# Kernel tuning notes

Hardware: AMD Instinct MI355X
Metric: run time of the kernel (lower is better)

## Reference

```python
import jax, jax.numpy as jnp
import numpy as np

B, S, HID, NH, FF, K = 2, 2048, 1024, 16, 4096, 512
DH = HID // NH


def setup_inputs() -> dict:
    key = jax.random.key(0)
    ks = jax.random.split(key, 24)
    w = lambda k, shape: (jax.random.normal(k, shape, jnp.float32) * 0.02)
    inp = {
        'x': jax.random.normal(ks[0], (B, S, HID), jnp.float32),
        'mask': jnp.ones((B, 1, 1, S), jnp.int32),
        'Wq': w(ks[1], (HID, HID)), 'bq': jnp.zeros((HID,), jnp.float32),
        'Wk': w(ks[2], (HID, HID)), 'bk': jnp.zeros((HID,), jnp.float32),
        'Wv': w(ks[3], (HID, HID)), 'bv': jnp.zeros((HID,), jnp.float32),
        'Wo': w(ks[4], (HID, HID)), 'bo': jnp.zeros((HID,), jnp.float32),
        'rel_emb': w(ks[5], (2 * K, HID)),
        'Wpk': w(ks[6], (HID, HID)), 'bpk': jnp.zeros((HID,), jnp.float32),
        'Wpq': w(ks[7], (HID, HID)), 'bpq': jnp.zeros((HID,), jnp.float32),
        'ln1_g': jnp.ones((HID,), jnp.float32), 'ln1_b': jnp.zeros((HID,), jnp.float32),
        'ln2_g': jnp.ones((HID,), jnp.float32), 'ln2_b': jnp.zeros((HID,), jnp.float32),
        'W1': w(ks[8], (HID, FF)), 'b1': jnp.zeros((FF,), jnp.float32),
        'W2': w(ks[9], (FF, HID)), 'b2': jnp.zeros((HID,), jnp.float32),
    }
    return inp


def _layernorm(x, g, b, eps=1e-6):
    m = jnp.mean(x, -1, keepdims=True)
    v = jnp.mean(jnp.square(x - m), -1, keepdims=True)
    return (x - m) * jax.lax.rsqrt(v + eps) * g + b


def _disentangled_attention(x, mask, Wq, bq, Wk, bk, Wv, bv, Wo, bo,
                            rel_emb, Wpk, bpk, Wpq, bpq):
    # content projections -> [B, NH, S, DH]
    def heads(t):
        return t.reshape(B, S, NH, DH).transpose(0, 2, 1, 3)
    q = heads(x @ Wq + bq)
    k = heads(x @ Wk + bk)
    v = heads(x @ Wv + bv)

    # relative position index: rel[i, j] = clip(i - j, -K, K-1) + K in [0, 2K)
    pos = jnp.arange(S)
    rel = jnp.clip(pos[:, None] - pos[None, :], -K, K - 1) + K  # [S, S]

    # projected relative-position embeddings -> [2K, NH, DH]
    pos_k = (rel_emb @ Wpk + bpk).reshape(2 * K, NH, DH)
    pos_q = (rel_emb @ Wpq + bpq).reshape(2 * K, NH, DH)

    # content-to-content
    c2c = jnp.einsum('bhid,bhjd->bhij', q, k)
    # content-to-position: gather over relative bucket per (i, j)
    c2p_att = jnp.einsum('bhid,rhd->bhir', q, pos_k)               # [B,NH,S,2K]
    c2p = jnp.take_along_axis(c2p_att, rel[None, None, :, :], axis=-1)
    # position-to-content: K_j . Q_r[delta(j, i)], gather then transpose
    p2c_att = jnp.einsum('bhjd,rhd->bhjr', k, pos_q)               # [B,NH,S,2K]
    p2c = jnp.take_along_axis(p2c_att, rel[None, None, :, :], axis=-1)
    p2c = p2c.transpose(0, 1, 3, 2)

    scale = 1.0 / jnp.sqrt(jnp.asarray(3 * DH, jnp.float32))
    scores = (c2c + c2p + p2c) * scale                             # [B,NH,S,S]
    scores = jnp.where(mask == 0, jnp.asarray(-1e9, scores.dtype), scores)
    attn = jax.nn.softmax(scores, axis=-1)

    out = jnp.einsum('bhij,bhjd->bhid', attn, v)
    out = out.transpose(0, 2, 1, 3).reshape(B, S, HID)
    return out @ Wo + bo


def reference(x, mask, Wq, bq, Wk, bk, Wv, bv, Wo, bo, rel_emb, Wpk, bpk,
              Wpq, bpq, ln1_g, ln1_b, ln2_g, ln2_b, W1, b1, W2, b2):
    # pre-norm sublayer 1: x + attn(LN(x))
    h = x + _disentangled_attention(_layernorm(x, ln1_g, ln1_b), mask,
                                    Wq, bq, Wk, bk, Wv, bv, Wo, bo,
                                    rel_emb, Wpk, bpk, Wpq, bpq)
    # pre-norm sublayer 2: h + FFN(LN(h)), GELU activation
    hn = _layernorm(h, ln2_g, ln2_b)
    ff = jax.nn.gelu(hn @ W1 + b1) @ W2 + b2
    return h + ff
```

## Files before the change

### kernel.cpp

```cpp
#include <hip/hip_runtime.h>
#include <cstdint>
#include <cstddef>

#define DEV __device__ __forceinline__

typedef __attribute__((ext_vector_type(4))) float  f32x4;
typedef __attribute__((ext_vector_type(4))) float  float4v;
typedef __attribute__((ext_vector_type(8))) short  s16x8;
typedef __attribute__((ext_vector_type(4))) short  s16x4;

static constexpr int BB = 2, SS = 2048, HIDN = 1024, NHH = 16, FFN = 4096, DH = 64;
static constexpr int TWOK = 1024;
static constexpr int HG = 8;
static constexpr float ATT_SCALE = 0.07216878364870322f;

DEV short f2bf(float f) {
  union { float f; uint32_t u; } v; v.f = f;
  uint32_t r = (v.u + 0x7fffu + ((v.u >> 16) & 1u)) >> 16;
  return (short)r;
}
DEV float bfu(unsigned short u) {
  union { uint32_t u; float f; } v; v.u = ((uint32_t)u) << 16; return v.f;
}
DEV int imin(int a, int b) { return a < b ? a : b; }
DEV int imax(int a, int b) { return a > b ? a : b; }

DEV void gl_lds16(const void* g, void* l) {
  __builtin_amdgcn_global_load_lds((const __attribute__((address_space(1))) void*)g,
                                   (__attribute__((address_space(3))) void*)l, 16, 0, 0);
}

#define MFMA16(a, b, c) __builtin_amdgcn_mfma_f32_16x16x32_bf16((a), (b), (c), 0, 0, 0)

__global__ __launch_bounds__(256) void k_tcast(const float* __restrict__ in,
                                               short* __restrict__ out, int R, int C) {
  __shared__ float t[32][33];
  const int bx = blockIdx.x * 32, by = blockIdx.y * 32;
  const int tx = threadIdx.x & 31, ty = threadIdx.x >> 5;
#pragma unroll
  for (int r = ty; r < 32; r += 8) t[r][tx] = in[(size_t)(by + r) * C + bx + tx];
  __syncthreads();
#pragma unroll
  for (int c = ty; c < 32; c += 8) out[(size_t)(bx + c) * R + by + tx] = f2bf(t[tx][c]);
}

struct TCBatch { const float* in[5]; short* out[5]; };
__global__ __launch_bounds__(256) void k_tcast5(TCBatch tc) {
  __shared__ float t[32][33];
  const float* in = tc.in[blockIdx.z];
  short* out = tc.out[blockIdx.z];
  const int bx = blockIdx.x * 32, by = blockIdx.y * 32;
  const int tx = threadIdx.x & 31, ty = threadIdx.x >> 5;
#pragma unroll
  for (int r = ty; r < 32; r += 8) t[r][tx] = in[(size_t)(by + r) * 1024 + bx + tx];
  __syncthreads();
#pragma unroll
  for (int c = ty; c < 32; c += 8) out[(size_t)(bx + c) * 1024 + by + tx] = f2bf(t[tx][c]);
}

__global__ __launch_bounds__(256) void k_cast(const float* __restrict__ in,
                                              short* __restrict__ out, int n4) {
  const int i = blockIdx.x * 256 + threadIdx.x;
  if (i < n4) {
    float4v v = ((const float4v*)in)[i];
    s16x4 o; o[0] = f2bf(v.x); o[1] = f2bf(v.y); o[2] = f2bf(v.z); o[3] = f2bf(v.w);
    ((s16x4*)out)[i] = o;
  }
}

__global__ __launch_bounds__(256) void k_ln(const float* __restrict__ x,
                                            const float* __restrict__ gw,
                                            const float* __restrict__ bw,
                                            short* __restrict__ out) {
  const int row = blockIdx.x, t = threadIdx.x, lane = t & 63, wv = t >> 6;
  __shared__ float red[8];
  const float4v v = ((const float4v*)(x + (size_t)row * HIDN))[t];
  float s = v.x + v.y + v.z + v.w;
#pragma unroll
  for (int d = 1; d < 64; d <<= 1) s += __shfl_xor(s, d, 64);
  if (lane == 0) red[wv] = s;
  __syncthreads();
  const float mean = (red[0] + red[1] + red[2] + red[3]) * (1.f / 1024.f);
  const float dx = v.x - mean, dy = v.y - mean, dz = v.z - mean, dw = v.w - mean;
  float s2 = dx * dx + dy * dy + dz * dz + dw * dw;
#pragma unroll
  for (int d = 1; d < 64; d <<= 1) s2 += __shfl_xor(s2, d, 64);
  if (lane == 0) red[4 + wv] = s2;
  __syncthreads();
  const float var = (red[4] + red[5] + red[6] + red[7]) * (1.f / 1024.f);
  const float rs = rsqrtf(var + 1e-6f);
  const float4v g4 = ((const float4v*)gw)[t], b4 = ((const float4v*)bw)[t];
  s16x4 o;
  o[0] = f2bf(dx * rs * g4.x + b4.x);
  o[1] = f2bf(dy * rs * g4.y + b4.y);
  o[2] = f2bf(dz * rs * g4.z + b4.z);
  o[3] = f2bf(dw * rs * g4.w + b4.w);
  ((s16x4*)(out + (size_t)row * HIDN))[t] = o;
}

DEV void gemm_main(const short* __restrict__ A, const short* __restrict__ Bt, int K,
                   int m0, int n0, int tid, int wm, int wn, int lr, int lg,
                   short* As, short* Bs, f32x4 acc[4][4]) {
  for (int k0 = 0; k0 < K; k0 += 32) {
#pragma unroll
    for (int c = tid; c < 512; c += 256) {
      const int row = c >> 2, col = (c & 3) * 8;
      gl_lds16(A + (size_t)(m0 + row) * K + k0 + col, (char*)As + c * 16);
      gl_lds16(Bt + (size_t)(n0 + row) * K + k0 + col, (char*)Bs + c * 16);
    }
    __syncthreads();
    s16x8 af[4], bf[4];
#pragma unroll
    for (int fi = 0; fi < 4; ++fi) af[fi] = *(const s16x8*)&As[(wm + fi * 16 + lr) * 32 + lg * 8];
#pragma unroll
    for (int fj = 0; fj < 4; ++fj) bf[fj] = *(const s16x8*)&Bs[(wn + fj * 16 + lr) * 32 + lg * 8];
#pragma unroll
    for (int fi = 0; fi < 4; ++fi)
#pragma unroll
      for (int fj = 0; fj < 4; ++fj) acc[fi][fj] = MFMA16(af[fi], bf[fj], acc[fi][fj]);
    __syncthreads();
  }
}

enum { OM_GELU = 0, OM_RESID = 1 };

template <int OM>
__global__ __launch_bounds__(256) void k_gemm(const short* __restrict__ A,
                                              const short* __restrict__ Bt,
                                              const float* __restrict__ bias,
                                              const float* __restrict__ resid,
                                              void* __restrict__ out,
                                              int M, int N, int K) {
  __shared__ short As[128 * 32];
  __shared__ short Bs[128 * 32];
  const int tid = threadIdx.x, lane = tid & 63, wave = tid >> 6;
  const int m0 = blockIdx.y * 128, n0 = blockIdx.x * 128;
  const int wm = (wave >> 1) * 64, wn = (wave & 1) * 64;
  const int lr = lane & 15, lg = lane >> 4;

  f32x4 acc[4][4];
#pragma unroll
  for (int i = 0; i < 4; ++i)
#pragma unroll
    for (int j = 0; j < 4; ++j) acc[i][j] = (f32x4){0.f, 0.f, 0.f, 0.f};
  gemm_main(A, Bt, K, m0, n0, tid, wm, wn, lr, lg, As, Bs, acc);

#pragma unroll
  for (int fi = 0; fi < 4; ++fi)
#pragma unroll
    for (int fj = 0; fj < 4; ++fj) {
      const int n = n0 + wn + fj * 16 + lr;
      const float bv = bias[n];
#pragma unroll
      for (int r = 0; r < 4; ++r) {
        const int m = m0 + wm + fi * 16 + lg * 4 + r;
        float v = acc[fi][fj][r] + bv;
        if constexpr (OM == OM_GELU) {
          const float z = 0.7978845608028654f * (v + 0.044715f * v * v * v);
          const float th = 1.f - 2.f / (1.f + __expf(2.f * z));
          ((short*)out)[(size_t)m * N + n] = f2bf(0.5f * v * (1.f + th));
        } else {
          ((float*)out)[(size_t)m * N + n] = v + resid[(size_t)m * N + n];
        }
      }
    }
}

__global__ __launch_bounds__(256) void k_gemm_qkv(const short* __restrict__ A,
                                                  const short* __restrict__ Bt,
                                                  const float* __restrict__ bq,
                                                  const float* __restrict__ bk,
                                                  const float* __restrict__ bv,
                                                  short* __restrict__ qo,
                                                  short* __restrict__ ko,
                                                  short* __restrict__ vo) {
  __shared__ short As[128 * 32];
  __shared__ short Bs[128 * 32];
  const int tid = threadIdx.x, lane = tid & 63, wave = tid >> 6;
  const int m0 = blockIdx.y * 128, n0 = blockIdx.x * 128;
  const int wm = (wave >> 1) * 64, wn = (wave & 1) * 64;
  const int lr = lane & 15, lg = lane >> 4;

  f32x4 acc[4][4];
#pragma unroll
  for (int i = 0; i < 4; ++i)
#pragma unroll
    for (int j = 0; j < 4; ++j) acc[i][j] = (f32x4){0.f, 0.f, 0.f, 0.f};
  gemm_main(A, Bt, 1024, m0, n0, tid, wm, wn, lr, lg, As, Bs, acc);

#pragma unroll
  for (int fi = 0; fi < 4; ++fi)
#pragma unroll
    for (int fj = 0; fj < 4; ++fj) {
      const int n = n0 + wn + fj * 16 + lr;
      const int proj = n >> 10, nn = n & 1023;
      const int hh = nn >> 6, dd = nn & 63;
      const float bvv = (proj == 0 ? bq : proj == 1 ? bk : bv)[nn];
#pragma unroll
      for (int r = 0; r < 4; ++r) {
        const int m = m0 + wm + fi * 16 + lg * 4 + r;
        const int b = m >> 11, s = m & (SS - 1);
        const float v = acc[fi][fj][r] + bvv;
        if (proj == 2)
          vo[(((size_t)b * NHH + hh) * DH + dd) * SS + s] = f2bf(v);
        else
          (proj == 0 ? qo : ko)[(((size_t)b * NHH + hh) * SS + s) * DH + dd] = f2bf(v);
      }
    }
}

__global__ __launch_bounds__(256) void k_gemm_pos(const short* __restrict__ A,
                                                  const short* __restrict__ Bt,
                                                  const float* __restrict__ bpk,
                                                  const float* __restrict__ bpq,
                                                  short* __restrict__ pko,
                                                  short* __restrict__ pqo) {
  __shared__ short As[128 * 32];
  __shared__ short Bs[128 * 32];
  const int tid = threadIdx.x, lane = tid & 63, wave = tid >> 6;
  const int m0 = blockIdx.y * 128, n0 = blockIdx.x * 128;
  const int wm = (wave >> 1) * 64, wn = (wave & 1) * 64;
  const int lr = lane & 15, lg = lane >> 4;

  f32x4 acc[4][4];
#pragma unroll
  for (int i = 0; i < 4; ++i)
#pragma unroll
    for (int j = 0; j < 4; ++j) acc[i][j] = (f32x4){0.f, 0.f, 0.f, 0.f};
  gemm_main(A, Bt, 1024, m0, n0, tid, wm, wn, lr, lg, As, Bs, acc);

#pragma unroll
  for (int fi = 0; fi < 4; ++fi)
#pragma unroll
    for (int fj = 0; fj < 4; ++fj) {
      const int n = n0 + wn + fj * 16 + lr;
      const int pos = n >> 10, nn = n & 1023;
      const int hh = nn >> 6, dd = nn & 63;
      const float bvv = (pos == 0 ? bpk : bpq)[nn];
      short* ob = pos == 0 ? pko : pqo;
#pragma unroll
      for (int r = 0; r < 4; ++r) {
        const int m = m0 + wm + fi * 16 + lg * 4 + r;
        ob[((size_t)hh * TWOK + m) * DH + dd] = f2bf(acc[fi][fj][r] + bvv);
      }
    }
}

__global__ __launch_bounds__(256) void k_posgemm(const short* __restrict__ qh,
                                                 const short* __restrict__ kh,
                                                 const short* __restrict__ posk,
                                                 const short* __restrict__ posq,
                                                 short* __restrict__ c2pO,
                                                 short* __restrict__ p2cD,
                                                 short* __restrict__ p2cE, int h0) {
  __shared__ short As[128 * 64];
  __shared__ short Bs[128 * 64];
  __shared__ short L[128 * 129];
  const int tid = threadIdx.x, lane = tid & 63, wave = tid >> 6;
  const int z = blockIdx.z;
  const int hl = z & (HG - 1), b = (z >> 3) & 1, isP = z >> 4;
  const int h = h0 + hl;
  const int bhl = b * HG + hl;
  const int m0 = blockIdx.y * 128, n0 = blockIdx.x * 128;
  const int wm = (wave >> 1) * 64, wn = (wave & 1) * 64;
  const int lr = lane & 15, lg = lane >> 4;
  const short* Ab = (isP ? kh : qh) + ((size_t)b * NHH + h) * SS * DH;
  const short* Pb = (isP ? posq : posk) + (size_t)h * TWOK * DH;

#pragma unroll
  for (int c = tid; c < 1024; c += 256) {
    const int row = c >> 3, col = (c & 7) * 8;
    gl_lds16(Ab + (size_t)(m0 + row) * DH + col, (char*)As + c * 16);
    gl_lds16(Pb + (size_t)(n0 + row) * DH + col, (char*)Bs + c * 16);
  }
  __syncthreads();

  f32x4 acc[4][4];
#pragma unroll
  for (int i = 0; i < 4; ++i)
#pragma unroll
    for (int j = 0; j < 4; ++j) acc[i][j] = (f32x4){0.f, 0.f, 0.f, 0.f};

#pragma unroll
  for (int ks = 0; ks < 2; ++ks) {
    s16x8 af[4], bf[4];
#pragma unroll
    for (int fi = 0; fi < 4; ++fi) af[fi] = *(const s16x8*)&As[(wm + fi * 16 + lr) * 64 + ks * 32 + lg * 8];
#pragma unroll
    for (int fj = 0; fj < 4; ++fj) bf[fj] = *(const s16x8*)&Bs[(wn + fj * 16 + lr) * 64 + ks * 32 + lg * 8];
#pragma unroll
    for (int fi = 0; fi < 4; ++fi)
#pragma unroll
      for (int fj = 0; fj < 4; ++fj) acc[fi][fj] = MFMA16(af[fi], bf[fj], acc[fi][fj]);
  }

  if (!isP) {
    short* ob = c2pO + (size_t)bhl * SS * TWOK;
#pragma unroll
    for (int fi = 0; fi < 4; ++fi)
#pragma unroll
      for (int fj = 0; fj < 4; ++fj) {
        const int n = n0 + wn + fj * 16 + lr;
#pragma unroll
        for (int r = 0; r < 4; ++r) {
          const int m = m0 + wm + fi * 16 + lg * 4 + r;
          ob[(size_t)m * TWOK + n] = f2bf(acc[fi][fj][r]);
        }
      }
  } else {
#pragma unroll
    for (int fi = 0; fi < 4; ++fi)
#pragma unroll
      for (int fj = 0; fj < 4; ++fj) {
        const int n = n0 + wn + fj * 16 + lr;
        const int nl = n - n0;
#pragma unroll
        for (int r = 0; r < 4; ++r) {
          const int m = m0 + wm + fi * 16 + lg * 4 + r;
          const int ml = m - m0;
          const short val = f2bf(acc[fi][fj][r]);
          L[ml * 129 + nl] = val;
          if (n == 0)        p2cE[((size_t)bhl * 2 + 0) * SS + m] = val;
          if (n == TWOK - 1) p2cE[((size_t)bhl * 2 + 1) * SS + m] = val;
        }
      }
    __syncthreads();
    const int nl = tid & 127, ty = tid >> 7;
    const int ibase = m0 - n0 + 385;
    short* pD = p2cD + (size_t)bhl * SS * TWOK;
    for (int p = 0; p < 128; ++p) {
      const int il = p * 2 + ty;
      if (il < 255) {
        const int ml = nl + il - 127;
        const int ig = ibase + il;
        if (ml >= 0 && ml < 128 && ig >= 0 && ig < SS)
          pD[(size_t)ig * TWOK + n0 + nl] = L[ml * 129 + nl];
      }
    }
  }
}

__global__ __launch_bounds__(256) void k_attn(const short* __restrict__ qh,
                                              const short* __restrict__ kh,
                                              const short* __restrict__ vT,
                                              const short* __restrict__ c2p,
                                              const short* __restrict__ p2cD,
                                              const short* __restrict__ p2cE,
                                              const int* __restrict__ mask,
                                              short* __restrict__ ao, int h0) {
  __shared__ char smem[4 * 16 * 68 * 4];
  __shared__ float Mm[4][16];
  __shared__ float Lm[4][16];
  float (*Om)[16][68] = (float(*)[16][68])smem;
  short (*Ps)[16][72] = (short(*)[16][72])smem;

  const int tid = threadIdx.x, lane = tid & 63, wv = tid >> 6;
  const int lr = lane & 15, lg = lane >> 4;

  const int bid = blockIdx.x;
  const int itile = bid & 127;
  const int hl = (bid >> 7) & (HG - 1);
  const int b = bid >> 10;
  const int h = h0 + hl;
  const int i0 = itile * 16;
  const size_t bhoff = ((size_t)b * NHH + h) * SS * DH;
  const size_t bhl = (size_t)b * HG + hl;
  const int jq0 = wv * (SS / 4);

  const short* qrow = qh + bhoff + (size_t)(i0 + lr) * DH + lg * 8;
  const s16x8 qa0 = *(const s16x8*)qrow;
  const s16x8 qa1 = *(const s16x8*)(qrow + 32);

  const unsigned short* c2prow[4];
  float cLoV[4], cHiV[4];
#pragma unroll
  for (int r = 0; r < 4; ++r) {
    c2prow[r] = (const unsigned short*)(c2p + (bhl * SS + (size_t)(i0 + lg * 4 + r)) * TWOK);
    cLoV[r] = bfu(c2prow[r][0]);
    cHiV[r] = bfu(c2prow[r][TWOK - 1]);
  }
  const ptrdiff_t pdelta = (const char*)p2cD - (const char*)c2p;
  const unsigned short* pE0 = (const unsigned short*)(p2cE + (bhl * 2 + 0) * SS);
  const unsigned short* pE1 = (const unsigned short*)(p2cE + (bhl * 2 + 1) * SS);

  const int dbase = i0 + lg * 4 - lr;

  f32x4 oacc[4];
  float mprev[4], lsum[4];
#pragma unroll
  for (int r = 0; r < 4; ++r) {
    mprev[r] = -1e30f; lsum[r] = 0.f; oacc[r] = (f32x4){0.f, 0.f, 0.f, 0.f};
  }

  for (int jt = 0; jt < SS / 4 / 64; ++jt) {
    const int j0 = jq0 + jt * 64;
    const int d0 = i0 - j0;

    f32x4 sacc[4];
#pragma unroll
    for (int fj = 0; fj < 4; ++fj) {
      const short* krow = kh + bhoff + (size_t)(j0 + fj * 16 + lr) * DH + lg * 8;
      const s16x8 k0 = *(const s16x8*)krow;
      const s16x8 k1 = *(const s16x8*)(krow + 32);
      f32x4 a = (f32x4){0.f, 0.f, 0.f, 0.f};
      a = MFMA16(qa0, k0, a);
      a = MFMA16(qa1, k1, a);
      sacc[fj] = a;
    }

    float pvv[4][4];
    if (d0 >= 576) {
#pragma unroll
      for (int fj = 0; fj < 4; ++fj) {
        const int jl = fj * 16 + lr;
        const bool ok = mask[(size_t)b * SS + j0 + jl] != 0;
        const float pe = bfu(pE0[j0 + jl]);
#pragma unroll
        for (int r = 0; r < 4; ++r) {
          const float s = (sacc[fj][r] + cHiV[r] + pe) * ATT_SCALE;
          pvv[fj][r] = ok ? s : -1e9f;
        }
      }
    } else if (d0 <= -528) {
#pragma unroll
      for (int fj = 0; fj < 4; ++fj) {
        const int jl = fj * 16 + lr;
        const bool ok = mask[(size_t)b * SS + j0 + jl] != 0;
        const float pe = bfu(pE1[j0 + jl]);
#pragma unroll
        for (int r = 0; r < 4; ++r) {
          const float s = (sacc[fj][r] + cLoV[r] + pe) * ATT_SCALE;
          pvv[fj][r] = ok ? s : -1e9f;
        }
      }
    } else {
#pragma unroll
      for (int fj = 0; fj < 4; ++fj) {
        const int jl = fj * 16 + lr;
        const bool ok = mask[(size_t)b * SS + j0 + jl] != 0;
        const float pe0 = bfu(pE0[j0 + jl]);
        const float pe1 = bfu(pE1[j0 + jl]);
        const int dl0 = dbase - fj * 16 - j0;
#pragma unroll
        for (int r = 0; r < 4; ++r) {
          const int dl = dl0 + r;
          const int cc = imin(imax(dl + 512, 0), 1023);
          const int raw = 512 - dl;
          const int cp = imin(imax(raw, 0), 1023);
          const unsigned short* pDrow =
              (const unsigned short*)((const char*)c2prow[r] + pdelta);
          float p2cv = bfu(pDrow[cp]);
          p2cv = raw < 0 ? pe0 : p2cv;
          p2cv = raw > 1023 ? pe1 : p2cv;
          const float s = (sacc[fj][r] + bfu(c2prow[r][cc]) + p2cv) * ATT_SCALE;
          pvv[fj][r] = ok ? s : -1e9f;
        }
      }
    }

#pragma unroll
    for (int r = 0; r < 4; ++r) {
      float m = fmaxf(fmaxf(pvv[0][r], pvv[1][r]), fmaxf(pvv[2][r], pvv[3][r]));
#pragma unroll
      for (int dd = 1; dd < 16; dd <<= 1) m = fmaxf(m, __shfl_xor(m, dd, 64));
      const float mnew = fmaxf(mprev[r], m);
      const float corr = __expf(mprev[r] - mnew);
      float rs = 0.f;
#pragma unroll
      for (int fj = 0; fj < 4; ++fj) { pvv[fj][r] = __expf(pvv[fj][r] - mnew); rs += pvv[fj][r]; }
#pragma unroll
      for (int dd = 1; dd < 16; dd <<= 1) rs += __shfl_xor(rs, dd, 64);
      lsum[r] = lsum[r] * corr + rs;
      mprev[r] = mnew;
#pragma unroll
      for (int fd = 0; fd < 4; ++fd) oacc[fd][r] *= corr;
    }

#pragma unroll
    for (int fj = 0; fj < 4; ++fj)
#pragma unroll
      for (int r = 0; r < 4; ++r)
        Ps[wv][lg * 4 + r][fj * 16 + lr] = f2bf(pvv[fj][r]);

    const s16x8 pa0 = *(const s16x8*)&Ps[wv][lr][lg * 8];
    const s16x8 pa1 = *(const s16x8*)&Ps[wv][lr][32 + lg * 8];
#pragma unroll
    for (int fd = 0; fd < 4; ++fd) {
      const short* vrow = vT + bhoff + (size_t)(fd * 16 + lr) * SS + j0 + lg * 8;
      const s16x8 v0 = *(const s16x8*)vrow;
      const s16x8 v1 = *(const s16x8*)(vrow + 32);
      oacc[fd] = MFMA16(pa0, v0, oacc[fd]);
      oacc[fd] = MFMA16(pa1, v1, oacc[fd]);
    }
  }

  __syncthreads();
#pragma unroll
  for (int fd = 0; fd < 4; ++fd)
#pragma unroll
    for (int r = 0; r < 4; ++r)
      Om[wv][lg * 4 + r][fd * 16 + lr] = oacc[fd][r];
  if (lr == 0) {
#pragma unroll
    for (int r = 0; r < 4; ++r) { Mm[wv][lg * 4 + r] = mprev[r]; Lm[wv][lg * 4 + r] = lsum[r]; }
  }
  __syncthreads();

#pragma unroll
  for (int r = 0; r < 4; ++r) {
    const int il = lg * 4 + r;
    float mt = fmaxf(fmaxf(Mm[0][il], Mm[1][il]), fmaxf(Mm[2][il], Mm[3][il]));
    float L = 0.f, o = 0.f;
#pragma unroll
    for (int w = 0; w < 4; ++w) {
      const float sc = __expf(Mm[w][il] - mt);
      L += Lm[w][il] * sc;
      o += Om[w][il][wv * 16 + lr] * sc;
    }
    ao[((size_t)b * SS + i0 + il) * HIDN + h * DH + wv * 16 + lr] = f2bf(o / L);
  }
}

extern "C" void kernel_launch(void* const* d_in, const int* in_sizes, int n_in,
                              void* d_out, int out_size, void* d_ws, size_t ws_size,
                              hipStream_t stream) {
  const float* x   = (const float*)d_in[0];
  const int* mask  = (const int*)d_in[1];
  const float* Wq  = (const float*)d_in[2];  const float* bq  = (const float*)d_in[3];
  const float* Wk  = (const float*)d_in[4];  const float* bk  = (const float*)d_in[5];
  const float* Wv  = (const float*)d_in[6];  const float* bv  = (const float*)d_in[7];
  const float* Wo  = (const float*)d_in[8];  const float* bo  = (const float*)d_in[9];
  const float* rel = (const float*)d_in[10];
  const float* Wpk = (const float*)d_in[11]; const float* bpk = (const float*)d_in[12];
  const float* Wpq = (const float*)d_in[13]; const float* bpq = (const float*)d_in[14];
  const float* g1  = (const float*)d_in[15]; const float* be1 = (const float*)d_in[16];
  const float* g2  = (const float*)d_in[17]; const float* be2 = (const float*)d_in[18];
  const float* W1  = (const float*)d_in[19]; const float* bf1 = (const float*)d_in[20];
  const float* W2  = (const float*)d_in[21]; const float* bf2 = (const float*)d_in[22];
  float* out = (float*)d_out;

  char* ws = (char*)d_ws;
  const size_t MB = (size_t)1 << 20;
  short* aoB   = (short*)(ws + 0 * MB);
  short* qhB   = (short*)(ws + 8 * MB);
  short* khB   = (short*)(ws + 16 * MB);
  short* vTB   = (short*)(ws + 24 * MB);
  short* poskB = (short*)(ws + 32 * MB);
  short* posqB = (short*)(ws + 34 * MB);
  short* xn    = (short*)(ws + 36 * MB);
  short* WqT   = (short*)(ws + 44 * MB);
  short* WkT   = (short*)(ws + 46 * MB);
  short* WvT   = (short*)(ws + 48 * MB);
  short* WpkT  = (short*)(ws + 50 * MB);
  short* WpqT  = (short*)(ws + 52 * MB);
  short* relbf = (short*)(ws + 54 * MB);
  short* c2pG  = (short*)(ws + 36 * MB);
  short* p2cDG = (short*)(ws + 100 * MB);
  short* p2cE  = (short*)(ws + 164 * MB);
  short* WoT   = (short*)(ws + 36 * MB);
  short* hnB   = (short*)(ws + 38 * MB);
  short* W1T   = (short*)(ws + 46 * MB);
  short* W2T   = (short*)(ws + 54 * MB);
  short* midB  = (short*)(ws + 62 * MB);
  (void)ws_size; (void)in_sizes; (void)n_in; (void)out_size;

  const int M = BB * SS;

  TCBatch tc;
  tc.in[0] = Wq;  tc.out[0] = WqT;
  tc.in[1] = Wk;  tc.out[1] = WkT;
  tc.in[2] = Wv;  tc.out[2] = WvT;
  tc.in[3] = Wpk; tc.out[3] = WpkT;
  tc.in[4] = Wpq; tc.out[4] = WpqT;
  k_tcast5<<<dim3(32, 32, 5), 256, 0, stream>>>(tc);
  k_cast<<<1024, 256, 0, stream>>>(rel, relbf, 1024 * 1024 / 4);
  k_ln<<<M, 256, 0, stream>>>(x, g1, be1, xn);

  k_gemm_qkv<<<dim3(24, 32), 256, 0, stream>>>(xn, WqT, bq, bk, bv, qhB, khB, vTB);
  k_gemm_pos<<<dim3(16, 8), 256, 0, stream>>>(relbf, WpkT, bpk, bpq, poskB, posqB);

  for (int g = 0; g < NHH / HG; ++g) {
    const int h0 = g * HG;
    k_posgemm<<<dim3(8, 16, 4 * HG), 256, 0, stream>>>(qhB, khB, poskB, posqB,
                                                       c2pG, p2cDG, p2cE, h0);
    k_attn<<<BB * HG * 128, 256, 0, stream>>>(qhB, khB, vTB, c2pG, p2cDG, p2cE, mask, aoB, h0);
  }

  k_tcast<<<dim3(32, 32), 256, 0, stream>>>(Wo, WoT, 1024, 1024);
  k_gemm<OM_RESID><<<dim3(8, 32), 256, 0, stream>>>(aoB, WoT, bo, x, out, M, 1024, 1024);
  k_ln<<<M, 256, 0, stream>>>(out, g2, be2, hnB);
  k_tcast<<<dim3(128, 32), 256, 0, stream>>>(W1, W1T, 1024, 4096);
  k_tcast<<<dim3(32, 128), 256, 0, stream>>>(W2, W2T, 4096, 1024);
  k_gemm<OM_GELU><<<dim3(32, 32), 256, 0, stream>>>(hnB, W1T, bf1, nullptr, midB, M, 4096, 1024);
  k_gemm<OM_RESID><<<dim3(8, 32), 256, 0, stream>>>(midB, W2T, bf2, out, out, M, 1024, 4096);
}
```

Measured before the change: 723.2 us.

## Process 32 query rows per attention block and vectorize p2c diagonal scatter

The attention kernel now handles two 16-row query sub-tiles per block, so each K and V fragment load is reused across 32 rows and the grid is halved. The p2c diagonal scatter in the position GEMM now writes 8 contiguous shorts per thread with vector stores instead of scalar per-element stores. In exchange, register pressure rises from doubled accumulators, which may reduce occupancy, and the far-low threshold changed from -528 to -544.

```diff
diff --git a/kernel.cpp b/kernel.cpp
--- a/kernel.cpp
+++ b/kernel.cpp
@@ -325,16 +325,33 @@
         }
       }
     __syncthreads();
-    const int nl = tid & 127, ty = tid >> 7;
+    const int ty = tid >> 4;
+    const int cx = (tid & 15) * 8;
     const int ibase = m0 - n0 + 385;
     short* pD = p2cD + (size_t)bhl * SS * TWOK;
-    for (int p = 0; p < 128; ++p) {
-      const int il = p * 2 + ty;
-      if (il < 255) {
-        const int ml = nl + il - 127;
-        const int ig = ibase + il;
-        if (ml >= 0 && ml < 128 && ig >= 0 && ig < SS)
-          pD[(size_t)ig * TWOK + n0 + nl] = L[ml * 129 + nl];
+    for (int p = 0; p < 16; ++p) {
+      const int il = p * 16 + ty;
+      if (il >= 255) continue;
+      const int ig = ibase + il;
+      if (ig < 0 || ig >= SS) continue;
+      const int lo = imax(0, 127 - il), hi = imin(127, 254 - il);
+      if (cx > hi || cx + 7 < lo) continue;
+      short* dst = pD + (size_t)ig * TWOK + n0 + cx;
+      const int mlb = cx + il - 127;
+      if (cx >= lo && cx + 7 <= hi) {
+        s16x4 t0, t1;
+#pragma unroll
+        for (int q = 0; q < 4; ++q) t0[q] = L[(mlb + q) * 129 + cx + q];
+#pragma unroll
+        for (int q = 0; q < 4; ++q) t1[q] = L[(mlb + 4 + q) * 129 + cx + 4 + q];
+        *(s16x4*)dst = t0;
+        *(s16x4*)(dst + 4) = t1;
+      } else {
+#pragma unroll
+        for (int q = 0; q < 8; ++q) {
+          const int nl = cx + q;
+          if (nl >= lo && nl <= hi) dst[q] = L[(mlb + q) * 129 + nl];
+        }
       }
     }
   }
@@ -348,177 +365,222 @@
                                               const short* __restrict__ p2cE,
                                               const int* __restrict__ mask,
                                               short* __restrict__ ao, int h0) {
-  __shared__ char smem[4 * 16 * 68 * 4];
-  __shared__ float Mm[4][16];
-  __shared__ float Lm[4][16];
-  float (*Om)[16][68] = (float(*)[16][68])smem;
-  short (*Ps)[16][72] = (short(*)[16][72])smem;
+  __shared__ char smem[4 * 32 * 68 * 4];
+  __shared__ float Mm[4][32];
+  __shared__ float Lm[4][32];
+  float (*Om)[32][68] = (float(*)[32][68])smem;
+  short (*Ps)[32][72] = (short(*)[32][72])smem;
 
   const int tid = threadIdx.x, lane = tid & 63, wv = tid >> 6;
   const int lr = lane & 15, lg = lane >> 4;
 
   const int bid = blockIdx.x;
-  const int itile = bid & 127;
-  const int hl = (bid >> 7) & (HG - 1);
-  const int b = bid >> 10;
+  const int itile = bid & 63;
+  const int hl = (bid >> 6) & (HG - 1);
+  const int b = bid >> 9;
   const int h = h0 + hl;
-  const int i0 = itile * 16;
+  const int i0 = itile * 32;
   const size_t bhoff = ((size_t)b * NHH + h) * SS * DH;
   const size_t bhl = (size_t)b * HG + hl;
   const int jq0 = wv * (SS / 4);
 
-  const short* qrow = qh + bhoff + (size_t)(i0 + lr) * DH + lg * 8;
-  const s16x8 qa0 = *(const s16x8*)qrow;
-  const s16x8 qa1 = *(const s16x8*)(qrow + 32);
-
-  const unsigned short* c2prow[4];
-  float cLoV[4], cHiV[4];
-#pragma unroll
-  for (int r = 0; r < 4; ++r) {
-    c2prow[r] = (const unsigned short*)(c2p + (bhl * SS + (size_t)(i0 + lg * 4 + r)) * TWOK);
-    cLoV[r] = bfu(c2prow[r][0]);
-    cHiV[r] = bfu(c2prow[r][TWOK - 1]);
-  }
-  const ptrdiff_t pdelta = (const char*)p2cD - (const char*)c2p;
+  s16x8 qf[2][2];
+#pragma unroll
+  for (int hf = 0; hf < 2; ++hf) {
+    const short* qrow = qh + bhoff + (size_t)(i0 + hf * 16 + lr) * DH + lg * 8;
+    qf[hf][0] = *(const s16x8*)qrow;
+    qf[hf][1] = *(const s16x8*)(qrow + 32);
+  }
+
+  const unsigned short* c2pb = (const unsigned short*)(c2p + bhl * SS * TWOK);
+  const unsigned short* pDb  = (const unsigned short*)(p2cD + bhl * SS * TWOK);
+  float cLoV[2][4], cHiV[2][4];
+#pragma unroll
+  for (int hf = 0; hf < 2; ++hf)
+#pragma unroll
+    for (int r = 0; r < 4; ++r) {
+      const size_t ro = (size_t)(i0 + hf * 16 + lg * 4 + r) * TWOK;
+      cLoV[hf][r] = bfu(c2pb[ro]);
+      cHiV[hf][r] = bfu(c2pb[ro + TWOK - 1]);
+    }
   const unsigned short* pE0 = (const unsigned short*)(p2cE + (bhl * 2 + 0) * SS);
   const unsigned short* pE1 = (const unsigned short*)(p2cE + (bhl * 2 + 1) * SS);
 
   const int dbase = i0 + lg * 4 - lr;
 
-  f32x4 oacc[4];
-  float mprev[4], lsum[4];
-#pragma unroll
-  for (int r = 0; r < 4; ++r) {
-    mprev[r] = -1e30f; lsum[r] = 0.f; oacc[r] = (f32x4){0.f, 0.f, 0.f, 0.f};
-  }
+  f32x4 oacc[2][4];
+  float mprev[2][4], lsum[2][4];
+#pragma unroll
+  for (int hf = 0; hf < 2; ++hf)
+#pragma unroll
+    for (int r = 0; r < 4; ++r) {
+      mprev[hf][r] = -1e30f; lsum[hf][r] = 0.f;
+      oacc[hf][r] = (f32x4){0.f, 0.f, 0.f, 0.f};
+    }
 
   for (int jt = 0; jt < SS / 4 / 64; ++jt) {
     const int j0 = jq0 + jt * 64;
     const int d0 = i0 - j0;
 
-    f32x4 sacc[4];
+    s16x8 kf0[4], kf1[4];
 #pragma unroll
     for (int fj = 0; fj < 4; ++fj) {
       const short* krow = kh + bhoff + (size_t)(j0 + fj * 16 + lr) * DH + lg * 8;
-      const s16x8 k0 = *(const s16x8*)krow;
-      const s16x8 k1 = *(const s16x8*)(krow + 32);
-      f32x4 a = (f32x4){0.f, 0.f, 0.f, 0.f};
-      a = MFMA16(qa0, k0, a);
-      a = MFMA16(qa1, k1, a);
-      sacc[fj] = a;
-    }
-
-    float pvv[4][4];
-    if (d0 >= 576) {
+      kf0[fj] = *(const s16x8*)krow;
+      kf1[fj] = *(const s16x8*)(krow + 32);
+    }
+
+    f32x4 sacc[2][4];
+#pragma unroll
+    for (int hf = 0; hf < 2; ++hf)
 #pragma unroll
       for (int fj = 0; fj < 4; ++fj) {
-        const int jl = fj * 16 + lr;
-        const bool ok = mask[(size_t)b * SS + j0 + jl] != 0;
-        const float pe = bfu(pE0[j0 + jl]);
-#pragma unroll
-        for (int r = 0; r < 4; ++r) {
-          const float s = (sacc[fj][r] + cHiV[r] + pe) * ATT_SCALE;
-          pvv[fj][r] = ok ? s : -1e9f;
+        f32x4 a = (f32x4){0.f, 0.f, 0.f, 0.f};
+        a = MFMA16(qf[hf][0], kf0[fj], a);
+        a = MFMA16(qf[hf][1], kf1[fj], a);
+        sacc[hf][fj] = a;
+      }
+
+    int mk[4]; float pe0v[4], pe1v[4];
+    const bool farHi = (d0 >= 576), farLo = (d0 <= -544);
+#pragma unroll
+    for (int fj = 0; fj < 4; ++fj) mk[fj] = mask[(size_t)b * SS + j0 + fj * 16 + lr];
+    if (farHi) {
+#pragma unroll
+      for (int fj = 0; fj < 4; ++fj) pe0v[fj] = bfu(pE0[j0 + fj * 16 + lr]);
+    } else if (farLo) {
+#pragma unroll
+      for (int fj = 0; fj < 4; ++fj) pe1v[fj] = bfu(pE1[j0 + fj * 16 + lr]);
+    } else {
+#pragma unroll
+      for (int fj = 0; fj < 4; ++fj) {
+        pe0v[fj] = bfu(pE0[j0 + fj * 16 + lr]);
+        pe1v[fj] = bfu(pE1[j0 + fj * 16 + lr]);
+      }
+    }
+
+#pragma unroll
+    for (int hf = 0; hf < 2; ++hf) {
+      float pvv[4][4];
+      if (farHi) {
+#pragma unroll
+        for (int fj = 0; fj < 4; ++fj) {
+          const bool ok = mk[fj] != 0;
+#pragma unroll
+          for (int r = 0; r < 4; ++r) {
+            const float s = (sacc[hf][fj][r] + cHiV[hf][r] + pe0v[fj]) * ATT_SCALE;
+            pvv[fj][r] = ok ? s : -1e9f;
+          }
         }
-      }
-    } else if (d0 <= -528) {
-#pragma unroll
-      for (int fj = 0; fj < 4; ++fj) {
-        const int jl = fj * 16 + lr;
-        const bool ok = mask[(size_t)b * SS + j0 + jl] != 0;
-        const float pe = bfu(pE1[j0 + jl]);
-#pragma unroll
-        for (int r = 0; r < 4; ++r) {
-          const float s = (sacc[fj][r] + cLoV[r] + pe) * ATT_SCALE;
-          pvv[fj][r] = ok ? s : -1e9f;
+      } else if (farLo) {
+#pragma unroll
+        for (int fj = 0; fj < 4; ++fj) {
+          const bool ok = mk[fj] != 0;
+#pragma unroll
+          for (int r = 0; r < 4; ++r) {
+            const float s = (sacc[hf][fj][r] + cLoV[hf][r] + pe1v[fj]) * ATT_SCALE;
+            pvv[fj][r] = ok ? s : -1e9f;
+          }
         }
-      }
-    } else {
-#pragma unroll
-      for (int fj = 0; fj < 4; ++fj) {
-        const int jl = fj * 16 + lr;
-        const bool ok = mask[(size_t)b * SS + j0 + jl] != 0;
-        const float pe0 = bfu(pE0[j0 + jl]);
-        const float pe1 = bfu(pE1[j0 + jl]);
-        const int dl0 = dbase - fj * 16 - j0;
-#pragma unroll
-        for (int r = 0; r < 4; ++r) {
-          const int dl = dl0 + r;
-          const int cc = imin(imax(dl + 512, 0), 1023);
-          const int raw = 512 - dl;
-          const int cp = imin(imax(raw, 0), 1023);
-          const unsigned short* pDrow =
-              (const unsigned short*)((const char*)c2prow[r] + pdelta);
-          float p2cv = bfu(pDrow[cp]);
-          p2cv = raw < 0 ? pe0 : p2cv;
-          p2cv = raw > 1023 ? pe1 : p2cv;
-          const float s = (sacc[fj][r] + bfu(c2prow[r][cc]) + p2cv) * ATT_SCALE;
-          pvv[fj][r] = ok ? s : -1e9f;
+      } else {
+#pragma unroll
+        for (int fj = 0; fj < 4; ++fj) {
+          const bool ok = mk[fj] != 0;
+          const int dl0 = dbase + hf * 16 - fj * 16 - j0;
+#pragma unroll
+          for (int r = 0; r < 4; ++r) {
+            const int dl = dl0 + r;
+            const int cc = imin(imax(dl + 512, 0), 1023);
+            const int raw = 512 - dl;
+            const int cp = imin(imax(raw, 0), 1023);
+            const size_t ro = (size_t)(i0 + hf * 16 + lg * 4 + r) * TWOK;
+            float p2cv = bfu(pDb[ro + cp]);
+            p2cv = raw < 0 ? pe0v[fj] : p2cv;
+            p2cv = raw > 1023 ? pe1v[fj] : p2cv;
+            const float s = (sacc[hf][fj][r] + bfu(c2pb[ro + cc]) + p2cv) * ATT_SCALE;
+            pvv[fj][r] = ok ? s : -1e9f;
+          }
         }
       }
-    }
-
-#pragma unroll
-    for (int r = 0; r < 4; ++r) {
-      float m = fmaxf(fmaxf(pvv[0][r], pvv[1][r]), fmaxf(pvv[2][r], pvv[3][r]));
-#pragma unroll
-      for (int dd = 1; dd < 16; dd <<= 1) m = fmaxf(m, __shfl_xor(m, dd, 64));
-      const float mnew = fmaxf(mprev[r], m);
-      const float corr = __expf(mprev[r] - mnew);
-      float rs = 0.f;
-#pragma unroll
-      for (int fj = 0; fj < 4; ++fj) { pvv[fj][r] = __expf(pvv[fj][r] - mnew); rs += pvv[fj][r]; }
-#pragma unroll
-      for (int dd = 1; dd < 16; dd <<= 1) rs += __shfl_xor(rs, dd, 64);
-      lsum[r] = lsum[r] * corr + rs;
-      mprev[r] = mnew;
-#pragma unroll
-      for (int fd = 0; fd < 4; ++fd) oacc[fd][r] *= corr;
-    }
-
-#pragma unroll
-    for (int fj = 0; fj < 4; ++fj)
-#pragma unroll
-      for (int r = 0; r < 4; ++r)
-        Ps[wv][lg * 4 + r][fj * 16 + lr] = f2bf(pvv[fj][r]);
-
-    const s16x8 pa0 = *(const s16x8*)&Ps[wv][lr][lg * 8];
-    const s16x8 pa1 = *(const s16x8*)&Ps[wv][lr][32 + lg * 8];
+
+#pragma unroll
+      for (int r = 0; r < 4; ++r) {
+        float m = fmaxf(fmaxf(pvv[0][r], pvv[1][r]), fmaxf(pvv[2][r], pvv[3][r]));
+#pragma unroll
+        for (int dd = 1; dd < 16; dd <<= 1) m = fmaxf(m, __shfl_xor(m, dd, 64));
+        const float mnew = fmaxf(mprev[hf][r], m);
+        const float corr = __expf(mprev[hf][r] - mnew);
+        float rs = 0.f;
+#pragma unroll
+        for (int fj = 0; fj < 4; ++fj) { pvv[fj][r] = __expf(pvv[fj][r] - mnew); rs += pvv[fj][r]; }
+#pragma unroll
+        for (int dd = 1; dd < 16; dd <<= 1) rs += __shfl_xor(rs, dd, 64);
+        lsum[hf][r] = lsum[hf][r] * corr + rs;
+        mprev[hf][r] = mnew;
+#pragma unroll
+        for (int fd = 0; fd < 4; ++fd) oacc[hf][fd] *= corr;
+      }
+
+#pragma unroll
+      for (int fj = 0; fj < 4; ++fj)
+#pragma unroll
+        for (int r = 0; r < 4; ++r)
+          Ps[wv][hf * 16 + lg * 4 + r][fj * 16 + lr] = f2bf(pvv[fj][r]);
+    }
+
+    s16x8 vf0[4], vf1[4];
 #pragma unroll
     for (int fd = 0; fd < 4; ++fd) {
       const short* vrow = vT + bhoff + (size_t)(fd * 16 + lr) * SS + j0 + lg * 8;
-      const s16x8 v0 = *(const s16x8*)vrow;
-      const s16x8 v1 = *(const s16x8*)(vrow + 32);
-      oacc[fd] = MFMA16(pa0, v0, oacc[fd]);
-      oacc[fd] = MFMA16(pa1, v1, oacc[fd]);
+      vf0[fd] = *(const s16x8*)vrow;
+      vf1[fd] = *(const s16x8*)(vrow + 32);
+    }
+#pragma unroll
+    for (int hf = 0; hf < 2; ++hf) {
+      const s16x8 pa0 = *(const s16x8*)&Ps[wv][hf * 16 + lr][lg * 8];
+      const s16x8 pa1 = *(const s16x8*)&Ps[wv][hf * 16 + lr][32 + lg * 8];
+#pragma unroll
+      for (int fd = 0; fd < 4; ++fd) {
+        oacc[hf][fd] = MFMA16(pa0, vf0[fd], oacc[hf][fd]);
+        oacc[hf][fd] = MFMA16(pa1, vf1[fd], oacc[hf][fd]);
+      }
     }
   }
 
   __syncthreads();
 #pragma unroll
-  for (int fd = 0; fd < 4; ++fd)
-#pragma unroll
-    for (int r = 0; r < 4; ++r)
-      Om[wv][lg * 4 + r][fd * 16 + lr] = oacc[fd][r];
+  for (int hf = 0; hf < 2; ++hf)
+#pragma unroll
+    for (int fd = 0; fd < 4; ++fd)
+#pragma unroll
+      for (int r = 0; r < 4; ++r)
+        Om[wv][hf * 16 + lg * 4 + r][fd * 16 + lr] = oacc[hf][fd][r];
   if (lr == 0) {
 #pragma unroll
-    for (int r = 0; r < 4; ++r) { Mm[wv][lg * 4 + r] = mprev[r]; Lm[wv][lg * 4 + r] = lsum[r]; }
+    for (int hf = 0; hf < 2; ++hf)
+#pragma unroll
+      for (int r = 0; r < 4; ++r) {
+        Mm[wv][hf * 16 + lg * 4 + r] = mprev[hf][r];
+        Lm[wv][hf * 16 + lg * 4 + r] = lsum[hf][r];
+      }
   }
   __syncthreads();
 
 #pragma unroll
-  for (int r = 0; r < 4; ++r) {
-    const int il = lg * 4 + r;
-    float mt = fmaxf(fmaxf(Mm[0][il], Mm[1][il]), fmaxf(Mm[2][il], Mm[3][il]));
-    float L = 0.f, o = 0.f;
-#pragma unroll
-    for (int w = 0; w < 4; ++w) {
-      const float sc = __expf(Mm[w][il] - mt);
-      L += Lm[w][il] * sc;
-      o += Om[w][il][wv * 16 + lr] * sc;
-    }
-    ao[((size_t)b * SS + i0 + il) * HIDN + h * DH + wv * 16 + lr] = f2bf(o / L);
-  }
+  for (int hf = 0; hf < 2; ++hf)
+#pragma unroll
+    for (int r = 0; r < 4; ++r) {
+      const int il = hf * 16 + lg * 4 + r;
+      float mt = fmaxf(fmaxf(Mm[0][il], Mm[1][il]), fmaxf(Mm[2][il], Mm[3][il]));
+      float L = 0.f, o = 0.f;
+#pragma unroll
+      for (int w = 0; w < 4; ++w) {
+        const float sc = __expf(Mm[w][il] - mt);
+        L += Lm[w][il] * sc;
+        o += Om[w][il][wv * 16 + lr] * sc;
+      }
+      ao[((size_t)b * SS + i0 + il) * HIDN + h * DH + wv * 16 + lr] = f2bf(o / L);
+    }
 }
 
 extern "C" void kernel_launch(void* const* d_in, const int* in_sizes, int n_in,
@@ -583,7 +645,7 @@
     const int h0 = g * HG;
     k_posgemm<<<dim3(8, 16, 4 * HG), 256, 0, stream>>>(qhB, khB, poskB, posqB,
                                                        c2pG, p2cDG, p2cE, h0);
-    k_attn<<<BB * HG * 128, 256, 0, stream>>>(qhB, khB, vTB, c2pG, p2cDG, p2cE, mask, aoB, h0);
+    k_attn<<<BB * HG * 64, 256, 0, stream>>>(qhB, khB, vTB, c2pG, p2cDG, p2cE, mask, aoB, h0);
   }
 
   k_tcast<<<dim3(32, 32), 256, 0, stream>>>(Wo, WoT, 1024, 1024);
```

Measured after the change: 758.0 us. 1.05x slower.

## Stage c2p/p2c rows and mask in LDS, use 8 waves in attention, vectorize p2c scatter

Applied to the files above, without the earlier changes.

The attention kernel now preloads the 16 c2p and p2cD rows for its i-tile, along with the mask and edge vectors, into dynamic LDS using global_load_lds. The per-element scattered global gathers then become LDS reads. The block grows to 512 threads with 8 waves, each covering half as many key tiles, and the final merge runs over 8 partials. The p2cD diagonal scatter in the posgemm kernel now writes 8-element vector stores instead of per-element stores. The large dynamic LDS footprint limits occupancy to one block per CU, and launching with about 117 KB of dynamic LDS may need an attribute to be allowed.

```diff
diff --git a/kernel.cpp b/kernel.cpp
--- a/kernel.cpp
+++ b/kernel.cpp
@@ -13,6 +13,15 @@
 static constexpr int TWOK = 1024;
 static constexpr int HG = 8;
 static constexpr float ATT_SCALE = 0.07216878364870322f;
+
+static constexpr int ROWB = 2056;
+static constexpr int OFF_C2P = 0;
+static constexpr int OFF_P2D = 32896;
+static constexpr int OFF_MSK = 65792;
+static constexpr int OFF_PE0 = 73984;
+static constexpr int OFF_PE1 = 78080;
+static constexpr int OFF_OVL = 82176;
+static constexpr int DYN_LDS = 116992;
 
 DEV short f2bf(float f) {
   union { float f; uint32_t u; } v; v.f = f;
@@ -325,22 +334,39 @@
         }
       }
     __syncthreads();
-    const int nl = tid & 127, ty = tid >> 7;
+    const int ty = tid >> 4;
+    const int cx = (tid & 15) * 8;
     const int ibase = m0 - n0 + 385;
     short* pD = p2cD + (size_t)bhl * SS * TWOK;
-    for (int p = 0; p < 128; ++p) {
-      const int il = p * 2 + ty;
-      if (il < 255) {
-        const int ml = nl + il - 127;
-        const int ig = ibase + il;
-        if (ml >= 0 && ml < 128 && ig >= 0 && ig < SS)
-          pD[(size_t)ig * TWOK + n0 + nl] = L[ml * 129 + nl];
-      }
-    }
-  }
-}
-
-__global__ __launch_bounds__(256) void k_attn(const short* __restrict__ qh,
+    for (int p = 0; p < 16; ++p) {
+      const int il = p * 16 + ty;
+      if (il >= 255) continue;
+      const int ig = ibase + il;
+      if (ig < 0 || ig >= SS) continue;
+      const int lo = imax(0, 127 - il), hi = imin(127, 254 - il);
+      if (cx > hi || cx + 7 < lo) continue;
+      short* dst = pD + (size_t)ig * TWOK + n0 + cx;
+      const int mlb = cx + il - 127;
+      if (cx >= lo && cx + 7 <= hi) {
+        s16x4 t0, t1;
+#pragma unroll
+        for (int q = 0; q < 4; ++q) t0[q] = L[(mlb + q) * 129 + cx + q];
+#pragma unroll
+        for (int q = 0; q < 4; ++q) t1[q] = L[(mlb + 4 + q) * 129 + cx + 4 + q];
+        *(s16x4*)dst = t0;
+        *(s16x4*)(dst + 4) = t1;
+      } else {
+#pragma unroll
+        for (int q = 0; q < 8; ++q) {
+          const int nl = cx + q;
+          if (nl >= lo && nl <= hi) dst[q] = L[(mlb + q) * 129 + nl];
+        }
+      }
+    }
+  }
+}
+
+__global__ __launch_bounds__(512) void k_attn(const short* __restrict__ qh,
                                               const short* __restrict__ kh,
                                               const short* __restrict__ vT,
                                               const short* __restrict__ c2p,
@@ -348,11 +374,16 @@
                                               const short* __restrict__ p2cE,
                                               const int* __restrict__ mask,
                                               short* __restrict__ ao, int h0) {
-  __shared__ char smem[4 * 16 * 68 * 4];
-  __shared__ float Mm[4][16];
-  __shared__ float Lm[4][16];
-  float (*Om)[16][68] = (float(*)[16][68])smem;
-  short (*Ps)[16][72] = (short(*)[16][72])smem;
+  extern __shared__ char dynL[];
+  char* c2pL = dynL + OFF_C2P;
+  char* p2dL = dynL + OFF_P2D;
+  const int* maskL = (const int*)(dynL + OFF_MSK);
+  const unsigned short* pE0L = (const unsigned short*)(dynL + OFF_PE0);
+  const unsigned short* pE1L = (const unsigned short*)(dynL + OFF_PE1);
+  float (*Om)[16][68] = (float(*)[16][68])(dynL + OFF_OVL);
+  short (*Ps)[16][72] = (short(*)[16][72])(dynL + OFF_OVL);
+  __shared__ float Mm[8][16];
+  __shared__ float Lm[8][16];
 
   const int tid = threadIdx.x, lane = tid & 63, wv = tid >> 6;
   const int lr = lane & 15, lg = lane >> 4;
@@ -365,23 +396,36 @@
   const int i0 = itile * 16;
   const size_t bhoff = ((size_t)b * NHH + h) * SS * DH;
   const size_t bhl = (size_t)b * HG + hl;
-  const int jq0 = wv * (SS / 4);
+  const int jq0 = wv * (SS / 8);
+
+  for (int u = tid; u < 2048; u += 512) {
+    const int ri = u >> 7, off = (u & 127) * 16;
+    gl_lds16((const char*)(c2p + (bhl * SS + (size_t)(i0 + ri)) * TWOK) + off,
+             c2pL + ri * ROWB + off);
+    gl_lds16((const char*)(p2cD + (bhl * SS + (size_t)(i0 + ri)) * TWOK) + off,
+             p2dL + ri * ROWB + off);
+  }
+  gl_lds16((const char*)(mask + (size_t)b * SS) + tid * 16, (char*)(dynL + OFF_MSK) + tid * 16);
+  if (tid < 256)
+    gl_lds16((const char*)(p2cE + (bhl * 2 + 0) * SS) + tid * 16, dynL + OFF_PE0 + tid * 16);
+  else
+    gl_lds16((const char*)(p2cE + (bhl * 2 + 1) * SS) + (tid - 256) * 16,
+             dynL + OFF_PE1 + (tid - 256) * 16);
 
   const short* qrow = qh + bhoff + (size_t)(i0 + lr) * DH + lg * 8;
   const s16x8 qa0 = *(const s16x8*)qrow;
   const s16x8 qa1 = *(const s16x8*)(qrow + 32);
 
-  const unsigned short* c2prow[4];
+  __syncthreads();
+
+  int rowoff[4];
   float cLoV[4], cHiV[4];
 #pragma unroll
   for (int r = 0; r < 4; ++r) {
-    c2prow[r] = (const unsigned short*)(c2p + (bhl * SS + (size_t)(i0 + lg * 4 + r)) * TWOK);
-    cLoV[r] = bfu(c2prow[r][0]);
-    cHiV[r] = bfu(c2prow[r][TWOK - 1]);
-  }
-  const ptrdiff_t pdelta = (const char*)p2cD - (const char*)c2p;
-  const unsigned short* pE0 = (const unsigned short*)(p2cE + (bhl * 2 + 0) * SS);
-  const unsigned short* pE1 = (const unsigned short*)(p2cE + (bhl * 2 + 1) * SS);
+    rowoff[r] = (lg * 4 + r) * ROWB;
+    cLoV[r] = bfu(*(const unsigned short*)(c2pL + rowoff[r]));
+    cHiV[r] = bfu(*(const unsigned short*)(c2pL + rowoff[r] + (TWOK - 1) * 2));
+  }
 
   const int dbase = i0 + lg * 4 - lr;
 
@@ -392,7 +436,7 @@
     mprev[r] = -1e30f; lsum[r] = 0.f; oacc[r] = (f32x4){0.f, 0.f, 0.f, 0.f};
   }
 
-  for (int jt = 0; jt < SS / 4 / 64; ++jt) {
+  for (int jt = 0; jt < SS / 8 / 64; ++jt) {
     const int j0 = jq0 + jt * 64;
     const int d0 = i0 - j0;
 
@@ -413,8 +457,8 @@
 #pragma unroll
       for (int fj = 0; fj < 4; ++fj) {
         const int jl = fj * 16 + lr;
-        const bool ok = mask[(size_t)b * SS + j0 + jl] != 0;
-        const float pe = bfu(pE0[j0 + jl]);
+        const bool ok = maskL[j0 + jl] != 0;
+        const float pe = bfu(pE0L[j0 + jl]);
 #pragma unroll
         for (int r = 0; r < 4; ++r) {
           const float s = (sacc[fj][r] + cHiV[r] + pe) * ATT_SCALE;
@@ -425,8 +469,8 @@
 #pragma unroll
       for (int fj = 0; fj < 4; ++fj) {
         const int jl = fj * 16 + lr;
-        const bool ok = mask[(size_t)b * SS + j0 + jl] != 0;
-        const float pe = bfu(pE1[j0 + jl]);
+        const bool ok = maskL[j0 + jl] != 0;
+        const float pe = bfu(pE1L[j0 + jl]);
 #pragma unroll
         for (int r = 0; r < 4; ++r) {
           const float s = (sacc[fj][r] + cLoV[r] + pe) * ATT_SCALE;
@@ -437,9 +481,9 @@
 #pragma unroll
       for (int fj = 0; fj < 4; ++fj) {
         const int jl = fj * 16 + lr;
-        const bool ok = mask[(size_t)b * SS + j0 + jl] != 0;
-        const float pe0 = bfu(pE0[j0 + jl]);
-        const float pe1 = bfu(pE1[j0 + jl]);
+        const bool ok = maskL[j0 + jl] != 0;
+        const float pe0 = bfu(pE0L[j0 + jl]);
+        const float pe1 = bfu(pE1L[j0 + jl]);
         const int dl0 = dbase - fj * 16 - j0;
 #pragma unroll
         for (int r = 0; r < 4; ++r) {
@@ -447,12 +491,11 @@
           const int cc = imin(imax(dl + 512, 0), 1023);
           const int raw = 512 - dl;
           const int cp = imin(imax(raw, 0), 1023);
-          const unsigned short* pDrow =
-              (const unsigned short*)((const char*)c2prow[r] + pdelta);
-          float p2cv = bfu(pDrow[cp]);
+          const float c2pv = bfu(*(const unsigned short*)(c2pL + rowoff[r] + cc * 2));
+          float p2cv = bfu(*(const unsigned short*)(p2dL + rowoff[r] + cp * 2));
           p2cv = raw < 0 ? pe0 : p2cv;
           p2cv = raw > 1023 ? pe1 : p2cv;
-          const float s = (sacc[fj][r] + bfu(c2prow[r][cc]) + p2cv) * ATT_SCALE;
+          const float s = (sacc[fj][r] + c2pv + p2cv) * ATT_SCALE;
           pvv[fj][r] = ok ? s : -1e9f;
         }
       }
@@ -506,18 +549,22 @@
   }
   __syncthreads();
 
-#pragma unroll
-  for (int r = 0; r < 4; ++r) {
-    const int il = lg * 4 + r;
-    float mt = fmaxf(fmaxf(Mm[0][il], Mm[1][il]), fmaxf(Mm[2][il], Mm[3][il]));
-    float L = 0.f, o = 0.f;
-#pragma unroll
-    for (int w = 0; w < 4; ++w) {
-      const float sc = __expf(Mm[w][il] - mt);
-      L += Lm[w][il] * sc;
-      o += Om[w][il][wv * 16 + lr] * sc;
-    }
-    ao[((size_t)b * SS + i0 + il) * HIDN + h * DH + wv * 16 + lr] = f2bf(o / L);
+  if (wv < 4) {
+#pragma unroll
+    for (int r = 0; r < 4; ++r) {
+      const int il = lg * 4 + r;
+      float mt = -1e30f;
+#pragma unroll
+      for (int w = 0; w < 8; ++w) mt = fmaxf(mt, Mm[w][il]);
+      float L = 0.f, o = 0.f;
+#pragma unroll
+      for (int w = 0; w < 8; ++w) {
+        const float sc = __expf(Mm[w][il] - mt);
+        L += Lm[w][il] * sc;
+        o += Om[w][il][wv * 16 + lr] * sc;
+      }
+      ao[((size_t)b * SS + i0 + il) * HIDN + h * DH + wv * 16 + lr] = f2bf(o / L);
+    }
   }
 }
 
@@ -583,7 +630,8 @@
     const int h0 = g * HG;
     k_posgemm<<<dim3(8, 16, 4 * HG), 256, 0, stream>>>(qhB, khB, poskB, posqB,
                                                        c2pG, p2cDG, p2cE, h0);
-    k_attn<<<BB * HG * 128, 256, 0, stream>>>(qhB, khB, vTB, c2pG, p2cDG, p2cE, mask, aoB, h0);
+    k_attn<<<BB * HG * 128, 512, DYN_LDS, stream>>>(qhB, khB, vTB, c2pG, p2cDG, p2cE,
+                                                    mask, aoB, h0);
   }
 
   k_tcast<<<dim3(32, 32), 256, 0, stream>>>(Wo, WoT, 1024, 1024);
```

Measured after the change: 714.7 us. Within noise of the previous version (-1.2%).
